# Kernel tuning notes

Measured on AMD Instinct MI355X. Metric: run time of the kernel, lower is better.

## Reference

```python
import math
import jax, jax.numpy as jnp
import numpy as np

WINDOW = (2, 7, 7)
SHIFT = (1, 3, 3)
NUM_HEADS = 4
DIM = 128
B, D, H, W = 1, 16, 112, 112  # divisible by window -> no padding, shift active


def _rel_coords_table():
    wd, wh, ww = WINDOW
    cd = np.arange(-(wd - 1), wd, dtype=np.float32)
    ch = np.arange(-(wh - 1), wh, dtype=np.float32)
    cw = np.arange(-(ww - 1), ww, dtype=np.float32)
    t = np.stack(np.meshgrid(cd, ch, cw, indexing='ij'), axis=-1)  # [2wd-1,2wh-1,2ww-1,3]
    t[..., 0] /= (wd - 1)
    t[..., 1] /= (wh - 1)
    t[..., 2] /= (ww - 1)
    t *= 8.0
    t = np.sign(t) * np.log2(np.abs(t) + 1.0) / 3.0
    return t.reshape(-1, 3)


def _rel_pos_index():
    wd, wh, ww = WINDOW
    coords = np.stack(np.meshgrid(np.arange(wd), np.arange(wh), np.arange(ww), indexing='ij'))
    cf = coords.reshape(3, -1)
    rc = (cf[:, :, None] - cf[:, None, :]).transpose(1, 2, 0)  # [N,N,3]
    rc[..., 0] += wd - 1
    rc[..., 1] += wh - 1
    rc[..., 2] += ww - 1
    rc[..., 0] *= (2 * wh - 1) * (2 * ww - 1)
    rc[..., 1] *= (2 * ww - 1)
    return rc.sum(-1).reshape(-1)


def _attn_mask(pd, ph, pw):
    wd, wh, ww = WINDOW
    sd, sh, sw = SHIFT
    m = np.zeros((pd, ph, pw), np.float32)
    cnt = 0
    for d in ((0, -wd), (-wd, -sd), (-sd, None)):
        for h in ((0, -wh), (-wh, -sh), (-sh, None)):
            for w in ((0, -ww), (-ww, -sw), (-sw, None)):
                m[d[0]:d[1], h[0]:h[1], w[0]:w[1]] = cnt
                cnt += 1
    nwin = (pd // wd) * (ph // wh) * (pw // ww)
    m = m.reshape(pd // wd, wd, ph // wh, wh, pw // ww, ww)
    m = m.transpose(0, 2, 4, 1, 3, 5).reshape(nwin, -1)  # [nWin, N]
    diff = m[:, None, :] - m[:, :, None]
    return np.where(diff != 0, -100.0, 0.0).astype(np.float32)


def setup_inputs() -> dict:
    key = jax.random.key(0)
    ks = jax.random.split(key, 5)
    C = DIM
    return {
        'x': jax.random.normal(ks[0], (B, D, H, W, C), jnp.float32),
        'qkv_weight': jax.random.normal(ks[1], (3 * C, C), jnp.float32) * 0.02,
        'qkv_bias': jnp.zeros((3 * C,), jnp.float32),
        'proj_weight': jax.random.normal(ks[2], (C, C), jnp.float32) * 0.02,
        'proj_bias': jnp.zeros((C,), jnp.float32),
        'logit_scale': jnp.full((NUM_HEADS, 1, 1), math.log(10.0), jnp.float32),
        'cpb_w1': jax.random.normal(ks[3], (512, 3), jnp.float32) * 0.02,
        'cpb_b1': jnp.zeros((512,), jnp.float32),
        'cpb_w2': jax.random.normal(ks[4], (NUM_HEADS, 512), jnp.float32) * 0.02,
    }


def reference(x, qkv_weight, qkv_bias, proj_weight, proj_bias, logit_scale, cpb_w1, cpb_b1, cpb_w2):
    wd, wh, ww = WINDOW
    sd, sh, sw = SHIFT
    b, d, h, w, C = x.shape
    N = wd * wh * ww
    hd = C // NUM_HEADS

    # --- continuous relative position bias (SwinV2) ---
    table = jnp.asarray(_rel_coords_table())              # [M, 3]
    hid = jax.nn.relu(table @ cpb_w1.T + cpb_b1)          # [M, 512]
    bias_tab = hid @ cpb_w2.T                             # [M, nH]
    idx = jnp.asarray(_rel_pos_index())                   # [N*N]
    rpb = bias_tab[idx].reshape(N, N, NUM_HEADS).transpose(2, 0, 1)
    rpb = 16.0 * jax.nn.sigmoid(rpb)                      # [nH, N, N]

    # zero middle third of qkv bias (cosine attention path)
    qkv_b = qkv_bias.at[C:2 * C].set(0.0)

    # --- shift + window partition (no padding: dims divisible) ---
    xs = jnp.roll(x, (-sd, -sh, -sw), axis=(1, 2, 3))
    nd, nh, nw = d // wd, h // wh, w // ww
    nwin = nd * nh * nw
    xw = xs.reshape(b, nd, wd, nh, wh, nw, ww, C)
    xw = xw.transpose(0, 1, 3, 5, 2, 4, 6, 7).reshape(b * nwin, N, C)

    # --- qkv + cosine attention ---
    qkv = (xw @ qkv_weight.T + qkv_b).reshape(b * nwin, N, 3, NUM_HEADS, hd)
    qkv = qkv.transpose(2, 0, 3, 1, 4)                    # [3, BW, nH, N, hd]
    q, k, v = qkv[0], qkv[1], qkv[2]
    qn = q / jnp.maximum(jnp.linalg.norm(q, axis=-1, keepdims=True), 1e-12)
    kn = k / jnp.maximum(jnp.linalg.norm(k, axis=-1, keepdims=True), 1e-12)
    attn = jnp.einsum('wnid,wnjd->wnij', qn, kn)          # [BW, nH, N, N]
    scale = jnp.exp(jnp.minimum(logit_scale, math.log(100.0)))  # [nH,1,1]
    attn = attn * scale[None] + rpb[None]

    # --- shift mask ---
    mask = jnp.asarray(_attn_mask(d, h, w))               # [nWin, N, N]
    attn = attn.reshape(b, nwin, NUM_HEADS, N, N) + mask[None, :, None]
    attn = jax.nn.softmax(attn.reshape(b * nwin, NUM_HEADS, N, N), axis=-1)

    out = jnp.einsum('wnij,wnjd->wind', attn, v).reshape(b * nwin, N, C)
    out = out @ proj_weight.T + proj_bias

    # --- reverse window partition + reverse shift ---
    out = out.reshape(b, nd, nh, nw, wd, wh, ww, C)
    out = out.transpose(0, 1, 4, 2, 5, 3, 6, 7).reshape(b, d, h, w, C)
    out = jnp.roll(out, (sd, sh, sw), axis=(1, 2, 3))
    return out
```

## Files before the change

### kernel.cpp

```cpp
#include <hip/hip_runtime.h>
#include <hip/hip_bf16.h>

typedef unsigned short u16;
typedef __attribute__((ext_vector_type(8))) short bf16x8;
typedef __attribute__((ext_vector_type(4))) float f32x4;

#define MFMA(a, b, c) __builtin_amdgcn_mfma_f32_16x16x32_bf16((a), (b), (c), 0, 0, 0)
#define LOG2E 1.4426950408889634f

__device__ __forceinline__ u16 f2b(float f) {
  __hip_bfloat16 h = __float2bfloat16(f);
  return __builtin_bit_cast(u16, h);
}
__device__ __forceinline__ float bu2f(u16 u) {
  union { unsigned u; float f; } v; v.u = ((unsigned)u) << 16; return v.f;
}
__device__ __forceinline__ u16 f2bu_sw(float f) {
  union { float f; unsigned u; } v; v.f = f;
  unsigned r = v.u + 0x7fffu + ((v.u >> 16) & 1u);
  return (u16)(r >> 16);
}
__device__ __forceinline__ int maskcode(int tok, int bd, int bh, int bw) {
  int d = tok / 49, rem = tok - d * 49, hh = rem / 7, w = rem - hh * 7;
  int rd = bd ? (d == 0 ? 1 : 2) : 0;
  int rh = bh ? (hh < 4 ? 1 : 2) : 0;
  int rw = bw ? (w < 4 ? 1 : 2) : 0;
  return rd * 9 + rh * 3 + rw;
}
__device__ __forceinline__ int tokbase(int tok, int id, int ih, int iw) {
  int d = tok / 49, rem = tok - d * 49, hh = rem / 7, w2 = rem - hh * 7;
  int pd = (id * 2 + d + 1) & 15;
  int ph = ih * 7 + hh + 3; if (ph >= 112) ph -= 112;
  int pw = iw * 7 + w2 + 3; if (pw >= 112) pw -= 112;
  return ((pd * 112 + ph) * 112 + pw) << 7;
}

__global__ void cpb_mlp(const float* __restrict__ w1, const float* __restrict__ b1,
                        const float* __restrict__ w2, float* __restrict__ btab) {
  const int m = blockIdx.x;
  const int k = threadIdx.x;
  const int i0 = m / 169, rm = m % 169, i1 = rm / 13, i2 = rm % 13;
  float c0 = (float)(i0 - 1) * 8.0f;
  float c1 = (float)(i1 - 6) * (8.0f / 6.0f);
  float c2 = (float)(i2 - 6) * (8.0f / 6.0f);
  float t0 = (c0 > 0.f ? 1.f : (c0 < 0.f ? -1.f : 0.f)) * log2f(fabsf(c0) + 1.f) * (1.f / 3.f);
  float t1 = (c1 > 0.f ? 1.f : (c1 < 0.f ? -1.f : 0.f)) * log2f(fabsf(c1) + 1.f) * (1.f / 3.f);
  float t2 = (c2 > 0.f ? 1.f : (c2 < 0.f ? -1.f : 0.f)) * log2f(fabsf(c2) + 1.f) * (1.f / 3.f);
  float hid = fmaxf(w1[k * 3 + 0] * t0 + w1[k * 3 + 1] * t1 + w1[k * 3 + 2] * t2 + b1[k], 0.f);
  __shared__ float red[4][8];
#pragma unroll
  for (int h = 0; h < 4; ++h) {
    float v = hid * w2[h * 512 + k];
    for (int mm = 1; mm < 64; mm <<= 1) v += __shfl_xor(v, mm);
    if ((k & 63) == 0) red[h][k >> 6] = v;
  }
  __syncthreads();
  if (k < 4) {
    float s = 0.f;
#pragma unroll
    for (int j = 0; j < 8; ++j) s += red[k][j];
    btab[m * 4 + k] = s;
  }
}

__global__ void build_rpbf(const float* __restrict__ btab, float* __restrict__ rpbf) {
  const int total = 8 * 4 * 7 * 7 * 64 * 4;
  int n = blockIdx.x * 256 + threadIdx.x;
  if (n >= total) return;
  int r = n & 3;
  int lane = (n >> 2) & 63;
  int q = n >> 8;
  int c = q % 7;
  int wv = (q / 7) % 7;
  int h = (q / 49) % 4;
  int combo = q / 196;
  int tokK = 16 * c + (lane >> 4) * 4 + r;
  int tokQ = 16 * wv + (lane & 15);
  float v;
  if (tokK >= 98) {
    v = -1e30f;
  } else if (tokQ >= 98) {
    v = 0.f;
  } else {
    int dq = tokQ / 49, rq = tokQ % 49, hq = rq / 7, wq = rq % 7;
    int dk = tokK / 49, rk = tokK % 49, hk = rk / 7, wk = rk % 7;
    int idx = (dq - dk + 1) * 169 + (hq - hk + 6) * 13 + (wq - wk + 6);
    float b = btab[idx * 4 + h];
    v = (16.f / (1.f + expf(-b))) * LOG2E;
    int bd = (combo >> 2) & 1, bh = (combo >> 1) & 1, bw = combo & 1;
    if (maskcode(tokQ, bd, bh, bw) != maskcode(tokK, bd, bh, bw)) v -= 144.269504f;
  }
  rpbf[n] = v;
}

__global__ void pack_wqkv(const float* __restrict__ qkvw, u16* __restrict__ dst) {
  int bid = blockIdx.x;
  int h = bid / 160, rem = bid % 160, blk = rem / 32, r = rem % 32;
  int srow = (blk < 2 ? 0 : (blk < 4 ? 128 : 256)) + h * 32 + r;
  bool lo = (blk == 1) || (blk == 3);
  int c = threadIdx.x;
  float v = (c < 128) ? qkvw[srow * 128 + c] : 0.f;
  u16 hi = f2bu_sw(v);
  u16 outv = lo ? f2bu_sw(v - bu2f(hi)) : hi;
  dst[h * 21760 + blk * 4352 + r * 136 + c] = outv;
}

__global__ void pack_wproj(const float* __restrict__ pw, u16* __restrict__ dst) {
  int c = blockIdx.x;
  int m = threadIdx.x;
  float v = (m < 128) ? pw[c * 128 + m] : 0.f;
  dst[c * 136 + m] = f2bu_sw(v);
}

#define QHI 0
#define QLO 4480
#define KHI 8960
#define KLO 13440
#define PB  0
#define VTB 15232
#define VIDX(d, t) (VTB + (d) * 128 + ((t) ^ (((d) & 7) << 3)))

template <bool BF16OUT>
__global__ __launch_bounds__(448, 7) void swin_attn(
    const float* __restrict__ xg, const float* __restrict__ qkvb,
    const float* __restrict__ lscale, const float* __restrict__ rpbf,
    const u16* __restrict__ wqkv, u16* __restrict__ aoutb, float* __restrict__ aoutf) {
  __shared__ u16 lds[19328];
  const int tid = threadIdx.x;
  const int wv = tid >> 6;
  const int l = tid & 63;
  const int l15 = l & 15;
  const int lg = l >> 4;
  const int bid = blockIdx.x;
  const int win = ((bid >> 5) << 3) | (bid & 7);
  const int h = (bid >> 3) & 3;
  const int iw = win & 15, ih = (win >> 4) & 15, id = win >> 8;
  const int combo = ((id == 7) << 2) | ((ih == 15) << 1) | (iw == 15);

  {
    const uint4* src = (const uint4*)(wqkv + h * 21760);
    uint4* dst = (uint4*)lds;
    for (int it = tid; it < 2176; it += 448) dst[it] = src[it];
  }
  const int arow = 16 * wv + l15;
  bf16x8 xa[4];
  {
    const int base = tokbase((arow < 98) ? arow : 0, id, ih, iw);
    const float* xp = xg + base + lg * 8;
#pragma unroll
    for (int ks = 0; ks < 4; ++ks) {
      const float4 a = *(const float4*)(xp + ks * 32);
      const float4 b4 = *(const float4*)(xp + ks * 32 + 4);
      u16* xo = (u16*)&xa[ks];
      xo[0] = f2b(a.x); xo[1] = f2b(a.y); xo[2] = f2b(a.z); xo[3] = f2b(a.w);
      xo[4] = f2b(b4.x); xo[5] = f2b(b4.y); xo[6] = f2b(b4.z); xo[7] = f2b(b4.w);
    }
  }
  __syncthreads();

  const f32x4 zf = {0.f, 0.f, 0.f, 0.f};
  f32x4 aq0 = zf, aq1 = zf, ak0 = zf, ak1 = zf, av0 = zf, av1 = zf;
  const u16* wvb = wqkv + h * 21760 + 17408 + lg * 8;
  bf16x8 bv0 = *(const bf16x8*)(wvb + l15 * 136);
  bf16x8 bv1 = *(const bf16x8*)(wvb + (16 + l15) * 136);
  __builtin_amdgcn_s_setprio(1);
#pragma unroll
  for (int ks = 0; ks < 4; ++ks) {
    const int k0 = ks * 32 + lg * 8;
    bf16x8 nv0, nv1;
    if (ks < 3) {
      nv0 = *(const bf16x8*)(wvb + l15 * 136 + (ks + 1) * 32);
      nv1 = *(const bf16x8*)(wvb + (16 + l15) * 136 + (ks + 1) * 32);
    }
    bf16x8 b;
    b = *(const bf16x8*)(&lds[l15 * 136 + k0]);                aq0 = MFMA(b, xa[ks], aq0);
    b = *(const bf16x8*)(&lds[4352 + l15 * 136 + k0]);         aq0 = MFMA(b, xa[ks], aq0);
    b = *(const bf16x8*)(&lds[(16 + l15) * 136 + k0]);         aq1 = MFMA(b, xa[ks], aq1);
    b = *(const bf16x8*)(&lds[4352 + (16 + l15) * 136 + k0]);  aq1 = MFMA(b, xa[ks], aq1);
    b = *(const bf16x8*)(&lds[8704 + l15 * 136 + k0]);         ak0 = MFMA(b, xa[ks], ak0);
    b = *(const bf16x8*)(&lds[13056 + l15 * 136 + k0]);        ak0 = MFMA(b, xa[ks], ak0);
    b = *(const bf16x8*)(&lds[8704 + (16 + l15) * 136 + k0]);  ak1 = MFMA(b, xa[ks], ak1);
    b = *(const bf16x8*)(&lds[13056 + (16 + l15) * 136 + k0]); ak1 = MFMA(b, xa[ks], ak1);
    av0 = MFMA(xa[ks], bv0, av0);
    av1 = MFMA(xa[ks], bv1, av1);
    if (ks < 3) { bv0 = nv0; bv1 = nv1; }
  }
  __builtin_amdgcn_s_setprio(0);
  __syncthreads();

  const f32x4* rbf = (const f32x4*)rpbf + (((combo * 4 + h) * 7 + wv) * 7) * 64 + l;
  f32x4 att[7];
#pragma unroll
  for (int c = 0; c < 7; ++c) att[c] = rbf[c * 64];

  const float sc2 = __expf(fminf(lscale[h], 4.60517019f)) * LOG2E;
  const float4 qb0v = *(const float4*)(qkvb + h * 32 + lg * 4);
  const float4 qb1v = *(const float4*)(qkvb + h * 32 + 16 + lg * 4);
  const float vb0 = qkvb[256 + h * 32 + l15];
  const float vb1 = qkvb[256 + h * 32 + 16 + l15];
  aq0[0] += qb0v.x; aq0[1] += qb0v.y; aq0[2] += qb0v.z; aq0[3] += qb0v.w;
  aq1[0] += qb1v.x; aq1[1] += qb1v.y; aq1[2] += qb1v.z; aq1[3] += qb1v.w;
#pragma unroll
  for (int r = 0; r < 4; ++r) { av0[r] += vb0; av1[r] += vb1; }
  float sq = 0.f, sk = 0.f;
#pragma unroll
  for (int r = 0; r < 4; ++r) {
    sq += aq0[r] * aq0[r] + aq1[r] * aq1[r];
    sk += ak0[r] * ak0[r] + ak1[r] * ak1[r];
  }
  sq += __shfl_xor(sq, 16); sq += __shfl_xor(sq, 32);
  sk += __shfl_xor(sk, 16); sk += __shfl_xor(sk, 32);
  const int tok = 16 * wv + l15;
  const bool ok = tok < 98;
  const float rnq = sc2 * rsqrtf(fmaxf(sq, 1e-24f));
  const float rnk = rsqrtf(fmaxf(sk, 1e-24f));
  {
    ushort4 qh0, qh1, ql0, ql1, kh0, kh1, kl0, kl1;
#pragma unroll
    for (int r = 0; r < 4; ++r) {
      float q0 = ok ? aq0[r] * rnq : 0.f;
      float q1 = ok ? aq1[r] * rnq : 0.f;
      float k0v = ok ? ak0[r] * rnk : 0.f;
      float k1v = ok ? ak1[r] * rnk : 0.f;
      u16 a = f2b(q0); ((u16*)&qh0)[r] = a; ((u16*)&ql0)[r] = f2b(q0 - bu2f(a));
      u16 b2 = f2b(q1); ((u16*)&qh1)[r] = b2; ((u16*)&ql1)[r] = f2b(q1 - bu2f(b2));
      u16 c2 = f2b(k0v); ((u16*)&kh0)[r] = c2; ((u16*)&kl0)[r] = f2b(k0v - bu2f(c2));
      u16 d2 = f2b(k1v); ((u16*)&kh1)[r] = d2; ((u16*)&kl1)[r] = f2b(k1v - bu2f(d2));
    }
    *(ushort4*)(&lds[QHI + tok * 40 + lg * 4]) = qh0;
    *(ushort4*)(&lds[QHI + tok * 40 + 16 + lg * 4]) = qh1;
    *(ushort4*)(&lds[QLO + tok * 40 + lg * 4]) = ql0;
    *(ushort4*)(&lds[QLO + tok * 40 + 16 + lg * 4]) = ql1;
    *(ushort4*)(&lds[KHI + tok * 40 + lg * 4]) = kh0;
    *(ushort4*)(&lds[KHI + tok * 40 + 16 + lg * 4]) = kh1;
    *(ushort4*)(&lds[KLO + tok * 40 + lg * 4]) = kl0;
    *(ushort4*)(&lds[KLO + tok * 40 + 16 + lg * 4]) = kl1;
  }
  __syncthreads();

  const bf16x8 qh = *(const bf16x8*)(&lds[QHI + tok * 40 + lg * 8]);
  const bf16x8 qlo = *(const bf16x8*)(&lds[QLO + tok * 40 + lg * 8]);
  __builtin_amdgcn_s_setprio(1);
#pragma unroll
  for (int c = 0; c < 7; ++c) {
    const bf16x8 kh = *(const bf16x8*)(&lds[KHI + (16 * c + l15) * 40 + lg * 8]);
    const bf16x8 kl = *(const bf16x8*)(&lds[KLO + (16 * c + l15) * 40 + lg * 8]);
    att[c] = MFMA(kh, qh, att[c]);
    att[c] = MFMA(kh, qlo, att[c]);
    att[c] = MFMA(kl, qh, att[c]);
  }
  __builtin_amdgcn_s_setprio(0);
  float s = 0.f;
#pragma unroll
  for (int c = 0; c < 7; ++c)
#pragma unroll
    for (int r = 0; r < 4; ++r) { float p = exp2f(att[c][r]); att[c][r] = p; s += p; }
  s += __shfl_xor(s, 16); s += __shfl_xor(s, 32);
  const float rsv = 1.0f / s;
  __syncthreads();

#pragma unroll
  for (int c = 0; c < 7; ++c) {
    ushort4 pk;
#pragma unroll
    for (int r = 0; r < 4; ++r) ((u16*)&pk)[r] = ok ? f2b(att[c][r]) : (u16)0;
    *(ushort4*)(&lds[PB + tok * 136 + 16 * c + lg * 4]) = pk;
  }
  {
    const int t0 = 16 * wv + lg * 4;
    ushort4 v0, v1;
    v0.x = (t0 + 0 < 98) ? f2b(av0[0]) : (u16)0;
    v0.y = (t0 + 1 < 98) ? f2b(av0[1]) : (u16)0;
    v0.z = (t0 + 2 < 98) ? f2b(av0[2]) : (u16)0;
    v0.w = (t0 + 3 < 98) ? f2b(av0[3]) : (u16)0;
    v1.x = (t0 + 0 < 98) ? f2b(av1[0]) : (u16)0;
    v1.y = (t0 + 1 < 98) ? f2b(av1[1]) : (u16)0;
    v1.z = (t0 + 2 < 98) ? f2b(av1[2]) : (u16)0;
    v1.w = (t0 + 3 < 98) ? f2b(av1[3]) : (u16)0;
    *(ushort4*)(&lds[VIDX(l15, t0)]) = v0;
    *(ushort4*)(&lds[VIDX(16 + l15, t0)]) = v1;
  }
  for (int it = tid; it < 32 * 16; it += 448) {
    int dd = it >> 4, t = 112 + (it & 15);
    lds[VIDX(dd, t)] = 0;
  }
  __syncthreads();

  f32x4 o0 = zf, o1 = zf;
  __builtin_amdgcn_s_setprio(1);
#pragma unroll
  for (int ks = 0; ks < 4; ++ks) {
    const int t = ks * 32 + lg * 8;
    const bf16x8 pb = *(const bf16x8*)(&lds[PB + tok * 136 + t]);
    const bf16x8 v0f = *(const bf16x8*)(&lds[VIDX(l15, t)]);
    const bf16x8 v1f = *(const bf16x8*)(&lds[VIDX(16 + l15, t)]);
    o0 = MFMA(v0f, pb, o0);
    o1 = MFMA(v1f, pb, o1);
  }
  __builtin_amdgcn_s_setprio(0);
  if (ok) {
    if (BF16OUT) {
      u16* ab = aoutb + (win * 98 + tok) * 128 + h * 32;
      ushort4 s0, s1;
      s0.x = f2b(o0[0] * rsv); s0.y = f2b(o0[1] * rsv);
      s0.z = f2b(o0[2] * rsv); s0.w = f2b(o0[3] * rsv);
      s1.x = f2b(o1[0] * rsv); s1.y = f2b(o1[1] * rsv);
      s1.z = f2b(o1[2] * rsv); s1.w = f2b(o1[3] * rsv);
      *(ushort4*)(ab + lg * 4) = s0;
      *(ushort4*)(ab + 16 + lg * 4) = s1;
    } else {
      float* ab = aoutf + tokbase(tok, id, ih, iw) + h * 32;
      f32x4 s0, s1;
#pragma unroll
      for (int r = 0; r < 4; ++r) { s0[r] = o0[r] * rsv; s1[r] = o1[r] * rsv; }
      *(f32x4*)(ab + lg * 4) = s0;
      *(f32x4*)(ab + 16 + lg * 4) = s1;
    }
  }
}

template <bool BF16OUT>
__global__ __launch_bounds__(448, 7) void swin_proj(const u16* __restrict__ wp,
                                                    const float* __restrict__ projb,
                                                    const u16* __restrict__ aoutb,
                                                    float* io) {
  __shared__ u16 w[17408];
  __shared__ int tb[98];
  const int tid = threadIdx.x;
  const int wv = tid >> 6;
  const int l = tid & 63;
  const int l15 = l & 15;
  const int lg = l >> 4;
  const int win = blockIdx.x;
  const int iw = win & 15, ih = (win >> 4) & 15, id = win >> 8;
  if (tid < 98) tb[tid] = tokbase(tid, id, ih, iw);
  {
    const uint4* src = (const uint4*)wp;
    uint4* dst = (uint4*)w;
    for (int it = tid; it < 2176; it += 448) dst[it] = src[it];
  }
  __syncthreads();
  const int tok = 16 * wv + l15;
  const int tokc = (tok < 98) ? tok : 97;

  const f32x4 zf = {0.f, 0.f, 0.f, 0.f};
  f32x4 pr[8];
#pragma unroll
  for (int n = 0; n < 8; ++n) pr[n] = zf;
#pragma unroll
  for (int ks = 0; ks < 4; ++ks) {
    bf16x8 oa;
    if (BF16OUT) {
      oa = *(const bf16x8*)(aoutb + (win * 98 + tokc) * 128 + ks * 32 + lg * 8);
    } else {
      const float* ap = io + tb[tokc] + ks * 32 + lg * 8;
      const float4 f0 = *(const float4*)(ap);
      const float4 f1 = *(const float4*)(ap + 4);
      u16* op = (u16*)&oa;
      op[0] = f2b(f0.x); op[1] = f2b(f0.y); op[2] = f2b(f0.z); op[3] = f2b(f0.w);
      op[4] = f2b(f1.x); op[5] = f2b(f1.y); op[6] = f2b(f1.z); op[7] = f2b(f1.w);
    }
#pragma unroll
    for (int n = 0; n < 8; ++n) {
      const bf16x8 wbf = *(const bf16x8*)(&w[(16 * n + l15) * 136 + ks * 32 + lg * 8]);
      pr[n] = MFMA(wbf, oa, pr[n]);
    }
  }
#pragma unroll
  for (int n = 0; n < 8; ++n) {
    const float4 pb4 = *(const float4*)(projb + 16 * n + lg * 4);
    f32x4 o = pr[n];
    o[0] += pb4.x; o[1] += pb4.y; o[2] += pb4.z; o[3] += pb4.w;
    if (tok < 98) *(f32x4*)(io + tb[tok] + 16 * n + lg * 4) = o;
  }
}

extern "C" void kernel_launch(void* const* d_in, const int* in_sizes, int n_in,
                              void* d_out, int out_size, void* d_ws, size_t ws_size,
                              hipStream_t stream) {
  const float* xg = (const float*)d_in[0];
  const float* qkvw = (const float*)d_in[1];
  const float* qkvb = (const float*)d_in[2];
  const float* projw = (const float*)d_in[3];
  const float* projb = (const float*)d_in[4];
  const float* lsc = (const float*)d_in[5];
  const float* w1 = (const float*)d_in[6];
  const float* b1 = (const float*)d_in[7];
  const float* w2 = (const float*)d_in[8];

  char* ws = (char*)d_ws;
  float* btab = (float*)(ws);
  u16* wq = (u16*)(ws + 8192);
  u16* wp = (u16*)(ws + 182272);
  float* rpbf = (float*)(ws + 217088);
  u16* aoutb = (u16*)(ws + 1822720);
  float* io = (float*)d_out;

  const bool bf16path = ws_size >= (size_t)53202944;

  cpb_mlp<<<507, 512, 0, stream>>>(w1, b1, w2, btab);
  build_rpbf<<<(8 * 4 * 7 * 7 * 64 * 4 + 255) / 256, 256, 0, stream>>>(btab, rpbf);
  pack_wqkv<<<640, 136, 0, stream>>>(qkvw, wq);
  pack_wproj<<<128, 136, 0, stream>>>(projw, wp);
  if (bf16path) {
    swin_attn<true><<<8192, 448, 0, stream>>>(xg, qkvb, lsc, rpbf, wq, aoutb, io);
    swin_proj<true><<<2048, 448, 0, stream>>>(wp, projb, aoutb, io);
  } else {
    swin_attn<false><<<8192, 448, 0, stream>>>(xg, qkvb, lsc, rpbf, wq, nullptr, io);
    swin_proj<false><<<2048, 448, 0, stream>>>(wp, projb, nullptr, io);
  }
}
```

Measured before the change: 179.6 us.

## Stream QKV weights from global in MFMA-friendly tiled layout, drop LDS staging

Repacks the per-head QKV weight into contiguous 32-wide k-slices so each lane's bf16x8 fragment can be read directly from global/L2, removing the block-wide copy of weights into shared memory and the two barriers around the QKV projection. The Q/K staging row stride is changed from 40 to 44 elements, presumably to reduce LDS bank conflicts, and the P-buffer write now zero-fills an eighth column chunk. This trades LDS traffic and synchronisation for more global/L2 loads per wave, which all 8192 blocks repeat.

```diff
diff --git a/kernel.cpp b/kernel.cpp
--- a/kernel.cpp
+++ b/kernel.cpp
@@ -99,10 +99,10 @@
   int srow = (blk < 2 ? 0 : (blk < 4 ? 128 : 256)) + h * 32 + r;
   bool lo = (blk == 1) || (blk == 3);
   int c = threadIdx.x;
-  float v = (c < 128) ? qkvw[srow * 128 + c] : 0.f;
+  float v = qkvw[srow * 128 + c];
   u16 hi = f2bu_sw(v);
   u16 outv = lo ? f2bu_sw(v - bu2f(hi)) : hi;
-  dst[h * 21760 + blk * 4352 + r * 136 + c] = outv;
+  dst[h * 20480 + blk * 4096 + (c >> 5) * 1024 + r * 32 + (c & 31)] = outv;
 }
 
 __global__ void pack_wproj(const float* __restrict__ pw, u16* __restrict__ dst) {
@@ -113,9 +113,9 @@
 }
 
 #define QHI 0
-#define QLO 4480
-#define KHI 8960
-#define KLO 13440
+#define QLO 4928
+#define KHI 9856
+#define KLO 14784
 #define PB  0
 #define VTB 15232
 #define VIDX(d, t) (VTB + (d) * 128 + ((t) ^ (((d) & 7) << 3)))
@@ -125,7 +125,7 @@
     const float* __restrict__ xg, const float* __restrict__ qkvb,
     const float* __restrict__ lscale, const float* __restrict__ rpbf,
     const u16* __restrict__ wqkv, u16* __restrict__ aoutb, float* __restrict__ aoutf) {
-  __shared__ u16 lds[19328];
+  __shared__ u16 lds[19712];
   const int tid = threadIdx.x;
   const int wv = tid >> 6;
   const int l = tid & 63;
@@ -137,11 +137,6 @@
   const int iw = win & 15, ih = (win >> 4) & 15, id = win >> 8;
   const int combo = ((id == 7) << 2) | ((ih == 15) << 1) | (iw == 15);
 
-  {
-    const uint4* src = (const uint4*)(wqkv + h * 21760);
-    uint4* dst = (uint4*)lds;
-    for (int it = tid; it < 2176; it += 448) dst[it] = src[it];
-  }
   const int arow = 16 * wv + l15;
   bf16x8 xa[4];
   {
@@ -156,37 +151,38 @@
       xo[4] = f2b(b4.x); xo[5] = f2b(b4.y); xo[6] = f2b(b4.z); xo[7] = f2b(b4.w);
     }
   }
-  __syncthreads();
 
   const f32x4 zf = {0.f, 0.f, 0.f, 0.f};
   f32x4 aq0 = zf, aq1 = zf, ak0 = zf, ak1 = zf, av0 = zf, av1 = zf;
-  const u16* wvb = wqkv + h * 21760 + 17408 + lg * 8;
-  bf16x8 bv0 = *(const bf16x8*)(wvb + l15 * 136);
-  bf16x8 bv1 = *(const bf16x8*)(wvb + (16 + l15) * 136);
-  __builtin_amdgcn_s_setprio(1);
-#pragma unroll
-  for (int ks = 0; ks < 4; ++ks) {
-    const int k0 = ks * 32 + lg * 8;
-    bf16x8 nv0, nv1;
-    if (ks < 3) {
-      nv0 = *(const bf16x8*)(wvb + l15 * 136 + (ks + 1) * 32);
-      nv1 = *(const bf16x8*)(wvb + (16 + l15) * 136 + (ks + 1) * 32);
-    }
-    bf16x8 b;
-    b = *(const bf16x8*)(&lds[l15 * 136 + k0]);                aq0 = MFMA(b, xa[ks], aq0);
-    b = *(const bf16x8*)(&lds[4352 + l15 * 136 + k0]);         aq0 = MFMA(b, xa[ks], aq0);
-    b = *(const bf16x8*)(&lds[(16 + l15) * 136 + k0]);         aq1 = MFMA(b, xa[ks], aq1);
-    b = *(const bf16x8*)(&lds[4352 + (16 + l15) * 136 + k0]);  aq1 = MFMA(b, xa[ks], aq1);
-    b = *(const bf16x8*)(&lds[8704 + l15 * 136 + k0]);         ak0 = MFMA(b, xa[ks], ak0);
-    b = *(const bf16x8*)(&lds[13056 + l15 * 136 + k0]);        ak0 = MFMA(b, xa[ks], ak0);
-    b = *(const bf16x8*)(&lds[8704 + (16 + l15) * 136 + k0]);  ak1 = MFMA(b, xa[ks], ak1);
-    b = *(const bf16x8*)(&lds[13056 + (16 + l15) * 136 + k0]); ak1 = MFMA(b, xa[ks], ak1);
-    av0 = MFMA(xa[ks], bv0, av0);
-    av1 = MFMA(xa[ks], bv1, av1);
-    if (ks < 3) { bv0 = nv0; bv1 = nv1; }
-  }
-  __builtin_amdgcn_s_setprio(0);
-  __syncthreads();
+  {
+    const u16* wb = wqkv + h * 20480 + lg * 8;
+    __builtin_amdgcn_s_setprio(1);
+#pragma unroll
+    for (int ks = 0; ks < 4; ++ks) {
+      const int o = ks * 1024;
+      bf16x8 b0 = *(const bf16x8*)(wb + o + l15 * 32);
+      bf16x8 b1 = *(const bf16x8*)(wb + 4096 + o + l15 * 32);
+      bf16x8 b2 = *(const bf16x8*)(wb + o + (16 + l15) * 32);
+      bf16x8 b3 = *(const bf16x8*)(wb + 4096 + o + (16 + l15) * 32);
+      bf16x8 b4 = *(const bf16x8*)(wb + 8192 + o + l15 * 32);
+      bf16x8 b5 = *(const bf16x8*)(wb + 12288 + o + l15 * 32);
+      bf16x8 b6 = *(const bf16x8*)(wb + 8192 + o + (16 + l15) * 32);
+      bf16x8 b7 = *(const bf16x8*)(wb + 12288 + o + (16 + l15) * 32);
+      bf16x8 b8 = *(const bf16x8*)(wb + 16384 + o + l15 * 32);
+      bf16x8 b9 = *(const bf16x8*)(wb + 16384 + o + (16 + l15) * 32);
+      aq0 = MFMA(b0, xa[ks], aq0);
+      aq0 = MFMA(b1, xa[ks], aq0);
+      aq1 = MFMA(b2, xa[ks], aq1);
+      aq1 = MFMA(b3, xa[ks], aq1);
+      ak0 = MFMA(b4, xa[ks], ak0);
+      ak0 = MFMA(b5, xa[ks], ak0);
+      ak1 = MFMA(b6, xa[ks], ak1);
+      ak1 = MFMA(b7, xa[ks], ak1);
+      av0 = MFMA(xa[ks], b8, av0);
+      av1 = MFMA(xa[ks], b9, av1);
+    }
+    __builtin_amdgcn_s_setprio(0);
+  }
 
   const f32x4* rbf = (const f32x4*)rpbf + (((combo * 4 + h) * 7 + wv) * 7) * 64 + l;
   f32x4 att[7];
@@ -227,24 +223,24 @@
       u16 c2 = f2b(k0v); ((u16*)&kh0)[r] = c2; ((u16*)&kl0)[r] = f2b(k0v - bu2f(c2));
       u16 d2 = f2b(k1v); ((u16*)&kh1)[r] = d2; ((u16*)&kl1)[r] = f2b(k1v - bu2f(d2));
     }
-    *(ushort4*)(&lds[QHI + tok * 40 + lg * 4]) = qh0;
-    *(ushort4*)(&lds[QHI + tok * 40 + 16 + lg * 4]) = qh1;
-    *(ushort4*)(&lds[QLO + tok * 40 + lg * 4]) = ql0;
-    *(ushort4*)(&lds[QLO + tok * 40 + 16 + lg * 4]) = ql1;
-    *(ushort4*)(&lds[KHI + tok * 40 + lg * 4]) = kh0;
-    *(ushort4*)(&lds[KHI + tok * 40 + 16 + lg * 4]) = kh1;
-    *(ushort4*)(&lds[KLO + tok * 40 + lg * 4]) = kl0;
-    *(ushort4*)(&lds[KLO + tok * 40 + 16 + lg * 4]) = kl1;
+    *(ushort4*)(&lds[QHI + tok * 44 + lg * 4]) = qh0;
+    *(ushort4*)(&lds[QHI + tok * 44 + 16 + lg * 4]) = qh1;
+    *(ushort4*)(&lds[QLO + tok * 44 + lg * 4]) = ql0;
+    *(ushort4*)(&lds[QLO + tok * 44 + 16 + lg * 4]) = ql1;
+    *(ushort4*)(&lds[KHI + tok * 44 + lg * 4]) = kh0;
+    *(ushort4*)(&lds[KHI + tok * 44 + 16 + lg * 4]) = kh1;
+    *(ushort4*)(&lds[KLO + tok * 44 + lg * 4]) = kl0;
+    *(ushort4*)(&lds[KLO + tok * 44 + 16 + lg * 4]) = kl1;
   }
   __syncthreads();
 
-  const bf16x8 qh = *(const bf16x8*)(&lds[QHI + tok * 40 + lg * 8]);
-  const bf16x8 qlo = *(const bf16x8*)(&lds[QLO + tok * 40 + lg * 8]);
+  const bf16x8 qh = *(const bf16x8*)(&lds[QHI + tok * 44 + lg * 8]);
+  const bf16x8 qlo = *(const bf16x8*)(&lds[QLO + tok * 44 + lg * 8]);
   __builtin_amdgcn_s_setprio(1);
 #pragma unroll
   for (int c = 0; c < 7; ++c) {
-    const bf16x8 kh = *(const bf16x8*)(&lds[KHI + (16 * c + l15) * 40 + lg * 8]);
-    const bf16x8 kl = *(const bf16x8*)(&lds[KLO + (16 * c + l15) * 40 + lg * 8]);
+    const bf16x8 kh = *(const bf16x8*)(&lds[KHI + (16 * c + l15) * 44 + lg * 8]);
+    const bf16x8 kl = *(const bf16x8*)(&lds[KLO + (16 * c + l15) * 44 + lg * 8]);
     att[c] = MFMA(kh, qh, att[c]);
     att[c] = MFMA(kh, qlo, att[c]);
     att[c] = MFMA(kl, qh, att[c]);
@@ -260,10 +256,11 @@
   __syncthreads();
 
 #pragma unroll
-  for (int c = 0; c < 7; ++c) {
+  for (int c = 0; c < 8; ++c) {
     ushort4 pk;
 #pragma unroll
-    for (int r = 0; r < 4; ++r) ((u16*)&pk)[r] = ok ? f2b(att[c][r]) : (u16)0;
+    for (int r = 0; r < 4; ++r)
+      ((u16*)&pk)[r] = (ok && c < 7) ? f2b(att[c < 7 ? c : 0][r]) : (u16)0;
     *(ushort4*)(&lds[PB + tok * 136 + 16 * c + lg * 4]) = pk;
   }
   {
@@ -391,16 +388,16 @@
   char* ws = (char*)d_ws;
   float* btab = (float*)(ws);
   u16* wq = (u16*)(ws + 8192);
-  u16* wp = (u16*)(ws + 182272);
-  float* rpbf = (float*)(ws + 217088);
-  u16* aoutb = (u16*)(ws + 1822720);
+  u16* wp = (u16*)(ws + 172032);
+  float* rpbf = (float*)(ws + 206848);
+  u16* aoutb = (u16*)(ws + 1812480);
   float* io = (float*)d_out;
 
-  const bool bf16path = ws_size >= (size_t)53202944;
+  const bool bf16path = ws_size >= (size_t)53192704;
 
   cpb_mlp<<<507, 512, 0, stream>>>(w1, b1, w2, btab);
   build_rpbf<<<(8 * 4 * 7 * 7 * 64 * 4 + 255) / 256, 256, 0, stream>>>(btab, rpbf);
-  pack_wqkv<<<640, 136, 0, stream>>>(qkvw, wq);
+  pack_wqkv<<<640, 128, 0, stream>>>(qkvw, wq);
   pack_wproj<<<128, 136, 0, stream>>>(projw, wp);
   if (bf16path) {
     swin_attn<true><<<8192, 448, 0, stream>>>(xg, qkvb, lsc, rpbf, wq, aoutb, io);
```

New measurement: 268.2 us. 1.49x slower.
